# Optimization experiments

Measured on AMD Instinct MI355X. Metric: run time of the kernel, lower is better.

The kernel has to match this reference:

```python
import jax, jax.numpy as jnp
import numpy as np

RADIUS = 0.12
K = 32  # neighbors per ball


def setup_inputs() -> dict:
    key = jax.random.key(0)
    ks = jax.random.split(key, 12)
    B, N, M, C = 4, 4096, 4096, 128
    anchor_xyzs = jax.random.uniform(ks[0], (B, N, 3), dtype=jnp.float32)
    neighbor = jax.random.uniform(ks[1], (B, M, 3), dtype=jnp.float32)
    s3 = 1.0 / np.sqrt(3.0)
    sC = 1.0 / np.sqrt(C)
    Wq = jax.random.uniform(ks[2], (3, C), jnp.float32, -s3, s3)
    bq = jax.random.uniform(ks[3], (C,), jnp.float32, -s3, s3)
    Wk = jax.random.uniform(ks[4], (3, C), jnp.float32, -s3, s3)
    bk = jax.random.uniform(ks[5], (C,), jnp.float32, -s3, s3)
    Wd = jax.random.uniform(ks[6], (3, C), jnp.float32, -s3, s3)
    bd = jax.random.uniform(ks[7], (C,), jnp.float32, -s3, s3)
    Wa = jax.random.uniform(ks[8], (C, C), jnp.float32, -sC, sC)
    ba = jax.random.uniform(ks[9], (C,), jnp.float32, -sC, sC)
    return {"anchor_xyzs": anchor_xyzs, "neighbor": neighbor,
            "Wq": Wq, "bq": bq, "Wk": Wk, "bk": bk,
            "Wd": Wd, "bd": bd, "Wa": Wa, "ba": ba}


def ball_query(anchor, neighbor, radius, k):
    """pointnet2-style ball query: first k neighbor indices (in original order)
    with sqdist < radius^2; slots beyond the found count are padded with the
    first found index (index 0 if none found). Returns (B, N, k) int32."""
    # (B, N, M) pairwise squared distances
    sqd = jnp.sum((anchor[:, :, None, :] - neighbor[:, None, :, :]) ** 2, axis=-1)
    mask = sqd < radius * radius
    # stable sort keys: valid (0) before invalid (1) -> first-k valid indices in order
    order = jnp.argsort((~mask).astype(jnp.int32), axis=-1, stable=True)
    idx = order[..., :k]                                # (B, N, k)
    cnt = jnp.sum(mask, axis=-1)                        # (B, N)
    slot_valid = jnp.arange(k) < cnt[..., None]
    idx = jnp.where(slot_valid, idx, idx[..., :1])
    return idx.astype(jnp.int32)


def reference(anchor_xyzs, neighbor, Wq, bq, Wk, bk, Wd, bd, Wa, ba):
    B, N, _ = anchor_xyzs.shape
    bidx = jnp.arange(B)[:, None, None]
    # QKV-style projections of coordinates
    Q = anchor_xyzs @ Wq + bq                           # (B, N, C)
    neighbor_k = neighbor @ Wk + bk                     # (B, M, C)
    # ball query + gather
    idx = ball_query(anchor_xyzs, neighbor, RADIUS, K)  # (B, N, K)
    neighbor_grouped = neighbor[bidx, idx]              # (B, N, K, 3)
    features_K = neighbor_k[bidx, idx]                  # (B, N, K, C)
    # distance encoding
    dis = (anchor_xyzs[:, :, None, :] - neighbor_grouped) @ Wd + bd  # (B, N, K, C)
    # attention weight: softmax over channel dim (dim=-1, as in the torch code)
    logits = (Q[:, :, None, :] - features_K) @ Wa + ba  # (B, N, K, C)
    attention_weight = jax.nn.softmax(logits, axis=-1)
    # max-pool over the K neighbor axis
    attention = jnp.max(dis * attention_weight, axis=2)  # (B, N, C)
    return attention
```

## Files before the change

### kernel.cpp

```cpp
#include <hip/hip_runtime.h>
#include <math.h>

#define BDIM 4
#define NDIM 4096
#define MDIM 4096
#define CDIM 128
#define KSEL 32
#define NCELL 64
#define CAP 128

typedef float v2f __attribute__((ext_vector_type(2)));

#define PRE_BYTES (7 * CDIM * 4)
#define STARTS_BYTES ((NCELL + 1) * BDIM * 4)
#define PTS4_OFF (PRE_BYTES + STARTS_BYTES)
#define WS_NEEDED (PTS4_OFF + (size_t)BDIM * MDIM * 16)

__device__ __forceinline__ float exp2_hw(float x) {
    float r;
    asm("v_exp_f32 %0, %1" : "=v"(r) : "v"(x));
    return r;
}

template <int CTRL, int MASK>
__device__ __forceinline__ float dpp_add(float x) {
    const int r = __builtin_amdgcn_update_dpp(0, __float_as_int(x), CTRL, MASK, 0xF, true);
    return x + __int_as_float(r);
}
#define DPP_QUAD_XOR1 0xB1
#define DPP_QUAD_XOR2 0x4E
#define DPP_ROW_HALF_MIRROR 0x141
#define DPP_ROW_MIRROR      0x140
#define DPP_ROW_BCAST15     0x142
#define DPP_ROW_BCAST31     0x143

__device__ __forceinline__ int rank_before(unsigned long long mk) {
    return __builtin_amdgcn_mbcnt_hi((unsigned)(mk >> 32),
                                     __builtin_amdgcn_mbcnt_lo((unsigned)mk, 0));
}

__device__ __forceinline__ int cell_of(float v) {
    int c = (int)(v * 4.0f);
    return c < 0 ? 0 : (c > 3 ? 3 : c);
}

__device__ __forceinline__ v2f splat(float x) { v2f r; r.x = x; r.y = x; return r; }

__device__ __forceinline__ v2f pk_fma(v2f a, v2f b, v2f c) {
    return __builtin_elementwise_fma(a, b, c);
}

struct LaneW {
    v2f wqa0, wqa1, wqa2;
    v2f nka0, nka1, nka2;
    v2f cav;
    v2f wd0, wd1, wd2, bdv;
};

__device__ __forceinline__ void load_lane_weights(LaneW& P, const float* pre,
                                                  const float* Wd, const float* bd, int lane) {
    const v2f* pre2 = (const v2f*)pre;
    const v2f* wdp  = (const v2f*)Wd;
    const v2f* bdp  = (const v2f*)bd;
    P.wqa0 = pre2[0 * 64 + lane]; P.wqa1 = pre2[1 * 64 + lane]; P.wqa2 = pre2[2 * 64 + lane];
    P.nka0 = pre2[3 * 64 + lane]; P.nka1 = pre2[4 * 64 + lane]; P.nka2 = pre2[5 * 64 + lane];
    P.cav  = pre2[6 * 64 + lane];
    P.wd0 = wdp[0 * 64 + lane]; P.wd1 = wdp[1 * 64 + lane]; P.wd2 = wdp[2 * 64 + lane];
    P.bdv = bdp[lane];
}

__device__ __forceinline__ void fold_one(int i, const float* Wq, const float* bq,
                                         const float* Wk, const float* bk,
                                         const float* Wa, const float* ba,
                                         float* pre) {
    const double LOG2E = 1.4426950408889634074;
    const int r = i >> 7, c = i & (CDIM - 1);
    if (r < 3) {
        double s0 = 0, s1 = 0, s2 = 0, s3 = 0;
        for (int k = 0; k < CDIM; k += 4) {
            s0 += (double)Wq[r * CDIM + k + 0] * (double)Wa[(k + 0) * CDIM + c];
            s1 += (double)Wq[r * CDIM + k + 1] * (double)Wa[(k + 1) * CDIM + c];
            s2 += (double)Wq[r * CDIM + k + 2] * (double)Wa[(k + 2) * CDIM + c];
            s3 += (double)Wq[r * CDIM + k + 3] * (double)Wa[(k + 3) * CDIM + c];
        }
        pre[r * CDIM + c] = (float)(((s0 + s1) + (s2 + s3)) * LOG2E);
    } else if (r < 6) {
        const int rr = r - 3;
        double s0 = 0, s1 = 0, s2 = 0, s3 = 0;
        for (int k = 0; k < CDIM; k += 4) {
            s0 += (double)Wk[rr * CDIM + k + 0] * (double)Wa[(k + 0) * CDIM + c];
            s1 += (double)Wk[rr * CDIM + k + 1] * (double)Wa[(k + 1) * CDIM + c];
            s2 += (double)Wk[rr * CDIM + k + 2] * (double)Wa[(k + 2) * CDIM + c];
            s3 += (double)Wk[rr * CDIM + k + 3] * (double)Wa[(k + 3) * CDIM + c];
        }
        pre[r * CDIM + c] = (float)(((s0 + s1) + (s2 + s3)) * (-LOG2E));
    } else {
        double s = (double)ba[c];
        for (int k = 0; k < CDIM; ++k)
            s += ((double)bq[k] - (double)bk[k]) * (double)Wa[k * CDIM + c];
        pre[6 * CDIM + c] = (float)(s * LOG2E);
    }
}

__launch_bounds__(1024)
__global__ void setup_kernel(const float* __restrict__ neighbor,
                             const float* __restrict__ Wq, const float* __restrict__ bq,
                             const float* __restrict__ Wk, const float* __restrict__ bk,
                             const float* __restrict__ Wa, const float* __restrict__ ba,
                             float* __restrict__ pre,
                             int* __restrict__ starts,
                             float4* __restrict__ pts4,
                             const int do_bins) {
    const int blk = blockIdx.x;
    const int t = threadIdx.x;
    if (do_bins && blk < BDIM) {
        __shared__ int cnts[NCELL];
        __shared__ int curs[NCELL];
        if (t < NCELL) cnts[t] = 0;
        __syncthreads();
        const float* nbb = neighbor + (size_t)blk * MDIM * 3;
        float px[4], py[4], pz[4];
        int cell[4];
        #pragma unroll
        for (int k = 0; k < 4; ++k) {
            const int i = t + k * 1024;
            const float x = nbb[3 * i], y = nbb[3 * i + 1], z = nbb[3 * i + 2];
            px[k] = x; py[k] = y; pz[k] = z;
            cell[k] = (cell_of(z) * 4 + cell_of(y)) * 4 + cell_of(x);
            atomicAdd(&cnts[cell[k]], 1);
        }
        __syncthreads();
        if (t < NCELL) {
            const int v = cnts[t];
            int inc = v;
            #pragma unroll
            for (int off = 1; off < 64; off <<= 1) {
                const int u = __shfl_up(inc, off);
                if (t >= off) inc += u;
            }
            const int excl = inc - v;
            curs[t] = excl;
            starts[blk * (NCELL + 1) + t] = excl;
            if (t == NCELL - 1) starts[blk * (NCELL + 1) + NCELL] = inc;
        }
        __syncthreads();
        #pragma unroll
        for (int k = 0; k < 4; ++k) {
            const int i = t + k * 1024;
            const int slot = atomicAdd(&curs[cell[k]], 1);
            pts4[(size_t)blk * MDIM + slot] = make_float4(px[k], py[k], pz[k], __int_as_float(i));
        }
    } else if (!do_bins || blk == BDIM) {
        if (t < 7 * CDIM) fold_one(t, Wq, bq, Wk, bk, Wa, ba, pre);
    }
}

__launch_bounds__(256, 6)
__global__ void attn2_kernel(const float* __restrict__ anchor,
                             const float* __restrict__ neighbor,
                             const float* __restrict__ Wd,
                             const float* __restrict__ bd,
                             const float* __restrict__ pre,
                             const float4* __restrict__ pts4,
                             const int* __restrict__ starts,
                             float* __restrict__ out) {
    __shared__ float4 cand[4][CAP - KSEL];
    __shared__ float4 sel[4][KSEL];

    const int b    = blockIdx.x >> 10;
    const int n0   = (blockIdx.x & 1023) << 2;
    const int tid  = threadIdx.x;
    const int w    = tid >> 6;
    const int lane = tid & 63;

    const int n = n0 + w;
    const float* ap = anchor + ((size_t)b * NDIM + n) * 3;
    const float ax = ap[0], ay = ap[1], az = ap[2];
    const float* nbb = neighbor + (size_t)b * MDIM * 3;

    LaneW P;
    load_lane_weights(P, pre, Wd, bd, lane);

    const v2f axv = splat(ax), ayv = splat(ay), azv = splat(az);
    const v2f qa  = pk_fma(axv, P.wqa0, pk_fma(ayv, P.wqa1, pk_fma(azv, P.wqa2, P.cav)));
    const v2f ad  = pk_fma(axv, P.wd0, pk_fma(ayv, P.wd1, pk_fma(azv, P.wd2, P.bdv)));
    const v2f nad = -ad;

    constexpr float R2 = (float)(0.12 * 0.12);
    const float RP = 0.1201f;

    const int cx0 = max(0, (int)((ax - RP) * 4.0f)), cx1 = min(3, (int)((ax + RP) * 4.0f));
    const int cy0 = max(0, (int)((ay - RP) * 4.0f)), cy1 = min(3, (int)((ay + RP) * 4.0f));
    const int cz0 = max(0, (int)((az - RP) * 4.0f)), cz1 = min(3, (int)((az + RP) * 4.0f));

    const float4* pb = pts4 + (size_t)b * MDIM;
    const int* st = starts + b * (NCELL + 1);

    const int r00 = (cz0 * 4 + cy0) * 4, r01 = (cz0 * 4 + cy1) * 4;
    const int r10 = (cz1 * 4 + cy0) * 4, r11 = (cz1 * 4 + cy1) * 4;
    int rs0 = st[r00 + cx0], re0 = st[r00 + cx1 + 1];
    int rs1 = st[r01 + cx0], re1 = st[r01 + cx1 + 1];
    int rs2 = st[r10 + cx0], re2 = st[r10 + cx1 + 1];
    int rs3 = st[r11 + cx0], re3 = st[r11 + cx1 + 1];
    const bool vy = cy1 > cy0, vz = cz1 > cz0;
    if (!vy) re1 = rs1;
    if (!vz) { re2 = rs2; re3 = rs3; }
    else if (!vy) re3 = rs3;

    int cnt = 0;
    auto scan_range = [&](int beg, int end) {
        for (int base = beg; base < end; base += 64) {
            const int i = base + lane;
            const float4 p = pb[min(i, end - 1)];
            const float dx = __fsub_rn(ax, p.x);
            const float dy = __fsub_rn(ay, p.y);
            const float dz = __fsub_rn(az, p.z);
            const float d2 = __fadd_rn(__fadd_rn(__fmul_rn(dx, dx), __fmul_rn(dy, dy)),
                                       __fmul_rn(dz, dz));
            const bool in = (i < end) && (d2 < R2);
            const unsigned long long mk = __ballot(in);
            const int pos = cnt + rank_before(mk);
            if (in && pos < CAP) {
                if (pos < KSEL) sel[w][pos] = p;
                else            cand[w][pos - KSEL] = p;
            }
            cnt += __popcll(mk);
        }
    };
    scan_range(rs0, re0);
    scan_range(rs1, re1);
    scan_range(rs2, re2);
    scan_range(rs3, re3);

    int eff;
    if (cnt == 0) {
        if (lane == 0) sel[w][0] = make_float4(nbb[0], nbb[1], nbb[2], 0.0f);
        eff = 1;
    } else if (cnt <= KSEL) {
        eff = cnt;
    } else if (cnt <= CAP) {
        float4 c0v = make_float4(0, 0, 0, 0), c1v = make_float4(0, 0, 0, 0);
        int i0 = 0x7fffffff, i1 = 0x7fffffff;
        if (lane < cnt) {
            c0v = (lane < KSEL) ? sel[w][lane] : cand[w][lane - KSEL];
            i0 = __float_as_int(c0v.w);
        }
        if (lane + 64 < cnt) {
            c1v = cand[w][lane + 64 - KSEL];
            i1 = __float_as_int(c1v.w);
        }
        int lo = 0, hi = MDIM - 1;
        while (lo < hi) {
            const int mid = (lo + hi) >> 1;
            const int c = __popcll(__ballot(i0 <= mid)) + __popcll(__ballot(i1 <= mid));
            if (c >= KSEL) hi = mid; else lo = mid + 1;
        }
        __builtin_amdgcn_wave_barrier();
        const bool k0 = (i0 <= lo);
        const unsigned long long m0 = __ballot(k0);
        if (k0) sel[w][rank_before(m0)] = c0v;
        const int cc0 = __popcll(m0);
        const bool k1 = (i1 <= lo);
        const unsigned long long m1 = __ballot(k1);
        if (k1) sel[w][cc0 + rank_before(m1)] = c1v;
        eff = KSEL;
    } else {
        int c2 = 0;
        for (int base = 0; base < MDIM && c2 < KSEL; base += 64) {
            const int m = base + lane;
            const float* p = nbb + 3 * m;
            const float nx = p[0], ny = p[1], nz = p[2];
            const float dx = __fsub_rn(ax, nx);
            const float dy = __fsub_rn(ay, ny);
            const float dz = __fsub_rn(az, nz);
            const float d2 = __fadd_rn(__fadd_rn(__fmul_rn(dx, dx), __fmul_rn(dy, dy)),
                                       __fmul_rn(dz, dz));
            const bool in = d2 < R2;
            const unsigned long long mk = __ballot(in);
            const int pos = c2 + rank_before(mk);
            if (in && pos < KSEL) sel[w][pos] = make_float4(nx, ny, nz, 0.0f);
            c2 += __popcll(mk);
        }
        eff = KSEL;
    }

    const int eff4 = (eff + 3) & ~3;
    __builtin_amdgcn_wave_barrier();
    __builtin_amdgcn_s_waitcnt(0);
    if (lane >= eff && lane < eff4) {
        const float4 f = sel[w][0];
        sel[w][lane] = f;
    }
    __builtin_amdgcn_wave_barrier();

    v2f acc = splat(1e30f);
    for (int j = 0; j < eff4; j += 4) {
        v2f pr[4];
        float sv[4];
        #pragma unroll
        for (int t = 0; t < 4; ++t) {
            const float4 v = sel[w][j + t];
            const v2f vx = splat(v.x), vy2 = splat(v.y), vz2 = splat(v.z);
            const v2f l = pk_fma(vx, P.nka0, pk_fma(vy2, P.nka1, pk_fma(vz2, P.nka2, qa)));
            v2f e; e.x = exp2_hw(l.x); e.y = exp2_hw(l.y);
            sv[t] = e.x + e.y;
            const v2f m = pk_fma(vx, P.wd0, pk_fma(vy2, P.wd1, pk_fma(vz2, P.wd2, nad)));
            pr[t] = m * e;
        }
        #pragma unroll
        for (int t = 0; t < 4; ++t) sv[t] = dpp_add<DPP_QUAD_XOR1, 0xF>(sv[t]);
        #pragma unroll
        for (int t = 0; t < 4; ++t) sv[t] = dpp_add<DPP_QUAD_XOR2, 0xF>(sv[t]);
        #pragma unroll
        for (int t = 0; t < 4; ++t) sv[t] = dpp_add<DPP_ROW_HALF_MIRROR, 0xF>(sv[t]);
        #pragma unroll
        for (int t = 0; t < 4; ++t) sv[t] = dpp_add<DPP_ROW_MIRROR, 0xF>(sv[t]);
        #pragma unroll
        for (int t = 0; t < 4; ++t) sv[t] = dpp_add<DPP_ROW_BCAST15, 0xA>(sv[t]);
        #pragma unroll
        for (int t = 0; t < 4; ++t) sv[t] = dpp_add<DPP_ROW_BCAST31, 0xC>(sv[t]);
        #pragma unroll
        for (int t = 0; t < 4; ++t) {
            const float tot = __int_as_float(__builtin_amdgcn_readlane(__float_as_int(sv[t]), 63));
            const v2f iv = splat(__builtin_amdgcn_rcpf(tot));
            acc = __builtin_elementwise_min(acc, pr[t] * iv);
        }
    }

    float2 o; o.x = -acc.x; o.y = -acc.y;
    ((float2*)out)[((size_t)b * NDIM + n) * 64 + lane] = o;
}

__launch_bounds__(256)
__global__ void attn_fallback(const float* __restrict__ anchor,
                              const float* __restrict__ neighbor,
                              const float* __restrict__ Wd,
                              const float* __restrict__ bd,
                              const float* __restrict__ pre,
                              float* __restrict__ out) {
    __shared__ float4 sel[4][KSEL];
    __shared__ int lists[4][KSEL];

    const int b = blockIdx.x >> 10, n0 = (blockIdx.x & 1023) << 2;
    const int tid = threadIdx.x, w = tid >> 6, lane = tid & 63;
    const int n = n0 + w;
    const float* ap = anchor + ((size_t)b * NDIM + n) * 3;
    const float ax = ap[0], ay = ap[1], az = ap[2];
    const float* nbb = neighbor + (size_t)b * MDIM * 3;

    LaneW P;
    load_lane_weights(P, pre, Wd, bd, lane);
    const v2f axv = splat(ax), ayv = splat(ay), azv = splat(az);
    const v2f qa = pk_fma(axv, P.wqa0, pk_fma(ayv, P.wqa1, pk_fma(azv, P.wqa2, P.cav)));
    const v2f ad = pk_fma(axv, P.wd0, pk_fma(ayv, P.wd1, pk_fma(azv, P.wd2, P.bdv)));
    const v2f nwd0 = -P.wd0, nwd1 = -P.wd1, nwd2 = -P.wd2;

    constexpr float R2 = (float)(0.12 * 0.12);
    int cnt = 0;
    for (int base = 0; base < MDIM && cnt < KSEL; base += 64) {
        const int m = base + lane;
        const float* p = nbb + 3 * m;
        const float dx = __fsub_rn(ax, p[0]);
        const float dy = __fsub_rn(ay, p[1]);
        const float dz = __fsub_rn(az, p[2]);
        const float d2 = __fadd_rn(__fadd_rn(__fmul_rn(dx, dx), __fmul_rn(dy, dy)),
                                   __fmul_rn(dz, dz));
        const bool in = d2 < R2;
        const unsigned long long mk = __ballot(in);
        const int pos = cnt + rank_before(mk);
        if (in && pos < KSEL) lists[w][pos] = m;
        cnt += __popcll(mk);
    }
    int eff = cnt < KSEL ? cnt : KSEL;
    if (cnt == 0) { if (lane == 0) lists[w][0] = 0; eff = 1; }
    const int eff4 = (eff + 3) & ~3;
    if (lane == 0) for (int j = eff; j < eff4; ++j) lists[w][j] = lists[w][0];
    __builtin_amdgcn_wave_barrier();
    if (lane < eff4) {
        const float* p = nbb + 3 * lists[w][lane];
        sel[w][lane] = make_float4(p[0], p[1], p[2], 0.f);
    }
    __builtin_amdgcn_wave_barrier();

    v2f acc = splat(-1e30f);
    for (int j = 0; j < eff4; j += 4) {
        v2f pr[4]; float sv[4];
        #pragma unroll
        for (int t = 0; t < 4; ++t) {
            const float4 v = sel[w][j + t];
            const v2f vx = splat(v.x), vy = splat(v.y), vz = splat(v.z);
            const v2f l = pk_fma(vx, P.nka0, pk_fma(vy, P.nka1, pk_fma(vz, P.nka2, qa)));
            v2f e; e.x = exp2_hw(l.x); e.y = exp2_hw(l.y);
            sv[t] = e.x + e.y;
            const v2f d = pk_fma(vx, nwd0, pk_fma(vy, nwd1, pk_fma(vz, nwd2, ad)));
            pr[t] = d * e;
        }
        #pragma unroll
        for (int t = 0; t < 4; ++t) sv[t] = dpp_add<DPP_QUAD_XOR1, 0xF>(sv[t]);
        #pragma unroll
        for (int t = 0; t < 4; ++t) sv[t] = dpp_add<DPP_QUAD_XOR2, 0xF>(sv[t]);
        #pragma unroll
        for (int t = 0; t < 4; ++t) sv[t] = dpp_add<DPP_ROW_HALF_MIRROR, 0xF>(sv[t]);
        #pragma unroll
        for (int t = 0; t < 4; ++t) sv[t] = dpp_add<DPP_ROW_MIRROR, 0xF>(sv[t]);
        #pragma unroll
        for (int t = 0; t < 4; ++t) sv[t] = dpp_add<DPP_ROW_BCAST15, 0xA>(sv[t]);
        #pragma unroll
        for (int t = 0; t < 4; ++t) sv[t] = dpp_add<DPP_ROW_BCAST31, 0xC>(sv[t]);
        #pragma unroll
        for (int t = 0; t < 4; ++t) {
            const float tot = __int_as_float(__builtin_amdgcn_readlane(__float_as_int(sv[t]), 63));
            const v2f iv = splat(__builtin_amdgcn_rcpf(tot));
            acc = __builtin_elementwise_max(acc, pr[t] * iv);
        }
    }
    float2 o; o.x = acc.x; o.y = acc.y;
    ((float2*)out)[((size_t)b * NDIM + n) * 64 + lane] = o;
}

extern "C" void kernel_launch(void* const* d_in, const int* in_sizes, int n_in,
                              void* d_out, int out_size, void* d_ws, size_t ws_size,
                              hipStream_t stream) {
    const float* anchor   = (const float*)d_in[0];
    const float* neighbor = (const float*)d_in[1];
    const float* Wq = (const float*)d_in[2];
    const float* bq = (const float*)d_in[3];
    const float* Wk = (const float*)d_in[4];
    const float* bk = (const float*)d_in[5];
    const float* Wd = (const float*)d_in[6];
    const float* bd = (const float*)d_in[7];
    const float* Wa = (const float*)d_in[8];
    const float* ba = (const float*)d_in[9];
    float* out = (float*)d_out;

    float* pre   = (float*)d_ws;
    int* starts  = (int*)((char*)d_ws + PRE_BYTES);
    float4* pts4 = (float4*)((char*)d_ws + PTS4_OFF);

    if (ws_size >= WS_NEEDED) {
        setup_kernel<<<dim3(BDIM + 1), dim3(1024), 0, stream>>>(
            neighbor, Wq, bq, Wk, bk, Wa, ba, pre, starts, pts4, 1);
        attn2_kernel<<<dim3(BDIM * NDIM / 4), dim3(256), 0, stream>>>(
            anchor, neighbor, Wd, bd, pre, pts4, starts, out);
    } else {
        setup_kernel<<<dim3(1), dim3(1024), 0, stream>>>(
            neighbor, Wq, bq, Wk, bk, Wa, ba, pre, starts, pts4, 0);
        attn_fallback<<<dim3(BDIM * NDIM / 4), dim3(256), 0, stream>>>(
            anchor, neighbor, Wd, bd, pre, out);
    }
}
```

Before: 113.7 us.

## Parallelize spatial binning across many blocks with global histogram and scatter kernels

Replaces the single-block-per-batch binning setup with a 64-block count kernel that builds per-batch cell histograms through global atomics. A last-block-done counter then runs the prefix scan, and a separate scatter kernel places points into the binned float4 array. The weight folding now runs in extra blocks of the count kernel. This spreads the serial setup over more CUs, at the cost of a memset, an extra kernel launch, global atomics, and non-deterministic slot order within each cell.

```diff
diff --git a/kernel.cpp b/kernel.cpp
--- a/kernel.cpp
+++ b/kernel.cpp
@@ -12,8 +12,15 @@
 typedef float v2f __attribute__((ext_vector_type(2)));
 
 #define PRE_BYTES (7 * CDIM * 4)
+#define STARTS_OFF PRE_BYTES
 #define STARTS_BYTES ((NCELL + 1) * BDIM * 4)
-#define PTS4_OFF (PRE_BYTES + STARTS_BYTES)
+#define CNTS_OFF (STARTS_OFF + STARTS_BYTES)
+#define CNTS_BYTES (BDIM * NCELL * 4)
+#define DONE_OFF (CNTS_OFF + CNTS_BYTES)
+#define DONE_BYTES 16
+#define CURS_OFF (DONE_OFF + DONE_BYTES)
+#define CURS_BYTES (BDIM * NCELL * 4)
+#define PTS4_OFF (CURS_OFF + CURS_BYTES)
 #define WS_NEEDED (PTS4_OFF + (size_t)BDIM * MDIM * 16)
 
 __device__ __forceinline__ float exp2_hw(float x) {
@@ -102,57 +109,86 @@
     }
 }
 
-__launch_bounds__(1024)
-__global__ void setup_kernel(const float* __restrict__ neighbor,
-                             const float* __restrict__ Wq, const float* __restrict__ bq,
-                             const float* __restrict__ Wk, const float* __restrict__ bk,
-                             const float* __restrict__ Wa, const float* __restrict__ ba,
-                             float* __restrict__ pre,
-                             int* __restrict__ starts,
-                             float4* __restrict__ pts4,
-                             const int do_bins) {
+#define CBLK_PER_B 16
+#define CNT_BLOCKS (BDIM * CBLK_PER_B)
+#define PTS_PER_CBLK (MDIM / CBLK_PER_B)
+
+__launch_bounds__(256)
+__global__ void setup_count(const float* __restrict__ neighbor,
+                            const float* __restrict__ Wq, const float* __restrict__ bq,
+                            const float* __restrict__ Wk, const float* __restrict__ bk,
+                            const float* __restrict__ Wa, const float* __restrict__ ba,
+                            float* __restrict__ pre,
+                            int* __restrict__ starts,
+                            int* __restrict__ cnts_g,
+                            int* __restrict__ curs_g,
+                            int* __restrict__ done) {
     const int blk = blockIdx.x;
     const int t = threadIdx.x;
-    if (do_bins && blk < BDIM) {
-        __shared__ int cnts[NCELL];
-        __shared__ int curs[NCELL];
-        if (t < NCELL) cnts[t] = 0;
+    if (blk < CNT_BLOCKS) {
+        __shared__ int hist[NCELL];
+        __shared__ int lastflag;
+        const int b = blk >> 4;
+        const int i = (blk & (CBLK_PER_B - 1)) * PTS_PER_CBLK + t;
+        if (t < NCELL) hist[t] = 0;
         __syncthreads();
-        const float* nbb = neighbor + (size_t)blk * MDIM * 3;
-        float px[4], py[4], pz[4];
-        int cell[4];
-        #pragma unroll
-        for (int k = 0; k < 4; ++k) {
-            const int i = t + k * 1024;
-            const float x = nbb[3 * i], y = nbb[3 * i + 1], z = nbb[3 * i + 2];
-            px[k] = x; py[k] = y; pz[k] = z;
-            cell[k] = (cell_of(z) * 4 + cell_of(y)) * 4 + cell_of(x);
-            atomicAdd(&cnts[cell[k]], 1);
-        }
+        const float* p = neighbor + ((size_t)b * MDIM + i) * 3;
+        const float x = p[0], y = p[1], z = p[2];
+        const int cell = (cell_of(z) * 4 + cell_of(y)) * 4 + cell_of(x);
+        atomicAdd(&hist[cell], 1);
         __syncthreads();
         if (t < NCELL) {
-            const int v = cnts[t];
+            const int h = hist[t];
+            if (h) atomicAdd(&cnts_g[b * NCELL + t], h);
+        }
+        __threadfence();
+        __syncthreads();
+        if (t == 0) lastflag = (atomicAdd(done, 1) == CNT_BLOCKS - 1);
+        __syncthreads();
+        if (lastflag) {
+            __threadfence();
+            const int w = t >> 6, lane = t & 63;
+            const int v = __hip_atomic_load(&cnts_g[w * NCELL + lane],
+                                            __ATOMIC_RELAXED, __HIP_MEMORY_SCOPE_AGENT);
             int inc = v;
             #pragma unroll
             for (int off = 1; off < 64; off <<= 1) {
                 const int u = __shfl_up(inc, off);
-                if (t >= off) inc += u;
+                if (lane >= off) inc += u;
             }
             const int excl = inc - v;
-            curs[t] = excl;
-            starts[blk * (NCELL + 1) + t] = excl;
-            if (t == NCELL - 1) starts[blk * (NCELL + 1) + NCELL] = inc;
-        }
-        __syncthreads();
-        #pragma unroll
-        for (int k = 0; k < 4; ++k) {
-            const int i = t + k * 1024;
-            const int slot = atomicAdd(&curs[cell[k]], 1);
-            pts4[(size_t)blk * MDIM + slot] = make_float4(px[k], py[k], pz[k], __int_as_float(i));
-        }
-    } else if (!do_bins || blk == BDIM) {
-        if (t < 7 * CDIM) fold_one(t, Wq, bq, Wk, bk, Wa, ba, pre);
-    }
+            starts[w * (NCELL + 1) + lane] = excl;
+            if (lane == NCELL - 1) starts[w * (NCELL + 1) + NCELL] = inc;
+            curs_g[w * NCELL + lane] = excl;
+        }
+    } else {
+        const int idx = (blk - CNT_BLOCKS) * 256 + t;
+        if (idx < 7 * CDIM) fold_one(idx, Wq, bq, Wk, bk, Wa, ba, pre);
+    }
+}
+
+__launch_bounds__(256)
+__global__ void setup_scatter(const float* __restrict__ neighbor,
+                              int* __restrict__ curs_g,
+                              float4* __restrict__ pts4) {
+    const int blk = blockIdx.x;
+    const int t = threadIdx.x;
+    const int b = blk >> 4;
+    const int i = (blk & (CBLK_PER_B - 1)) * PTS_PER_CBLK + t;
+    const float* p = neighbor + ((size_t)b * MDIM + i) * 3;
+    const float x = p[0], y = p[1], z = p[2];
+    const int cell = (cell_of(z) * 4 + cell_of(y)) * 4 + cell_of(x);
+    const int slot = atomicAdd(&curs_g[b * NCELL + cell], 1);
+    pts4[(size_t)b * MDIM + slot] = make_float4(x, y, z, __int_as_float(i));
+}
+
+__launch_bounds__(1024)
+__global__ void setup_kernel(const float* __restrict__ Wq, const float* __restrict__ bq,
+                             const float* __restrict__ Wk, const float* __restrict__ bk,
+                             const float* __restrict__ Wa, const float* __restrict__ ba,
+                             float* __restrict__ pre) {
+    const int t = threadIdx.x;
+    if (t < 7 * CDIM) fold_one(t, Wq, bq, Wk, bk, Wa, ba, pre);
 }
 
 __launch_bounds__(256, 6)
@@ -434,17 +470,23 @@
     float* out = (float*)d_out;
 
     float* pre   = (float*)d_ws;
-    int* starts  = (int*)((char*)d_ws + PRE_BYTES);
+    int* starts  = (int*)((char*)d_ws + STARTS_OFF);
+    int* cnts_g  = (int*)((char*)d_ws + CNTS_OFF);
+    int* done    = (int*)((char*)d_ws + DONE_OFF);
+    int* curs_g  = (int*)((char*)d_ws + CURS_OFF);
     float4* pts4 = (float4*)((char*)d_ws + PTS4_OFF);
 
     if (ws_size >= WS_NEEDED) {
-        setup_kernel<<<dim3(BDIM + 1), dim3(1024), 0, stream>>>(
-            neighbor, Wq, bq, Wk, bk, Wa, ba, pre, starts, pts4, 1);
+        hipMemsetAsync((char*)d_ws + CNTS_OFF, 0, CNTS_BYTES + DONE_BYTES, stream);
+        setup_count<<<dim3(CNT_BLOCKS + 4), dim3(256), 0, stream>>>(
+            neighbor, Wq, bq, Wk, bk, Wa, ba, pre, starts, cnts_g, curs_g, done);
+        setup_scatter<<<dim3(CNT_BLOCKS), dim3(256), 0, stream>>>(
+            neighbor, curs_g, pts4);
         attn2_kernel<<<dim3(BDIM * NDIM / 4), dim3(256), 0, stream>>>(
             anchor, neighbor, Wd, bd, pre, pts4, starts, out);
     } else {
         setup_kernel<<<dim3(1), dim3(1024), 0, stream>>>(
-            neighbor, Wq, bq, Wk, bk, Wa, ba, pre, starts, pts4, 0);
+            Wq, bq, Wk, bk, Wa, ba, pre);
         attn_fallback<<<dim3(BDIM * NDIM / 4), dim3(256), 0, stream>>>(
             anchor, neighbor, Wd, bd, pre, out);
     }
```

Result: slower. 122.1 us (+7.4%).
